# Kernel tuning notes

Measured on AMD Instinct MI355X. Metric: run time of the kernel, lower is better.

## Reference

```python
import jax, jax.numpy as jnp
import numpy as np
from jax import lax

N_HEADS = 8
D_KEYS = 128
HALF = D_KEYS // 2
N_KEYS = 256          # sub-keys per set; n_experts = N_KEYS**2
TOP_K = 8
D_MODEL = 512


def setup_inputs() -> dict:
    key = jax.random.key(0)
    ks = jax.random.split(key, 6)
    N, T = 2, 1024
    queries = jax.random.normal(ks[0], (N, T, D_MODEL), dtype=jnp.float32)
    Wq = jax.random.normal(ks[1], (D_MODEL, N_HEADS * D_KEYS), dtype=jnp.float32) / np.sqrt(D_MODEL)
    bq = jnp.zeros((N_HEADS * D_KEYS,), dtype=jnp.float32)
    bound = 1.0 / np.sqrt(HALF)
    keys = jax.random.uniform(ks[2], (N_HEADS, 2, N_KEYS, HALF), dtype=jnp.float32,
                              minval=-bound, maxval=bound)
    w_down = jax.random.normal(ks[3], (N_KEYS * N_KEYS, D_MODEL), dtype=jnp.float32) * 0.02
    w_up = jax.random.normal(ks[4], (N_KEYS * N_KEYS, D_MODEL), dtype=jnp.float32) * 0.02
    return {"queries": queries, "Wq": Wq, "bq": bq, "keys": keys,
            "w_down": w_down, "w_up": w_up}


def _forward(queries, Wq, bq, keys, w_down, w_up):
    N, T, D = queries.shape
    x = queries.reshape(-1, D)                                   # [B, D], B = N*T
    q = (x @ Wq + bq).reshape(-1, N_HEADS, D_KEYS)               # [B, H, d_keys]

    # product-key routing: score each half-query against each sub-key set
    q1, q2 = q[..., :HALF], q[..., HALF:]
    s1 = jnp.einsum('bhc,hnc->bhn', q1, keys[:, 0])              # [B, H, n_keys]
    s2 = jnp.einsum('bhc,hnc->bhn', q2, keys[:, 1])
    s1t, i1 = lax.top_k(s1, TOP_K)                               # [B, H, k]
    s2t, i2 = lax.top_k(s2, TOP_K)

    # cartesian product of the two top-k sets, then re-top-k
    all_scores = (s1t[..., :, None] + s2t[..., None, :]).reshape(-1, N_HEADS, TOP_K * TOP_K)
    all_idx = (i1[..., :, None] * N_KEYS + i2[..., None, :]).reshape(-1, N_HEADS, TOP_K * TOP_K)
    scores, best = lax.top_k(all_scores, TOP_K)                  # [B, H, k]
    indices = jnp.take_along_axis(all_idx, best, axis=-1)        # [B, H, k]

    # gather per-token expert weights and combine (PEER single-neuron experts)
    w_d = w_down[indices]                                        # [B, H, k, D]
    w_u = w_up[indices]                                          # [B, H, k, D]
    inner = jnp.einsum('bd,bhkd->bhk', x, w_d)                   # [B, H, k]
    vals = jax.nn.relu(inner) * jax.nn.softmax(scores, axis=-1)
    out = jnp.einsum('bhk,bhkd->bd', vals, w_u)                  # [B, D]
    return out.reshape(N, T, D)


def reference(queries, Wq, bq, keys, w_down, w_up):
    return _forward(queries, Wq, bq, keys, w_down, w_up)
```

## Files before the change

### kernel.cpp

```cpp
#include <hip/hip_runtime.h>
#include <math.h>

#define D_MODEL 512
#define NH      8
#define DK      128
#define HALFD   64
#define NKEYS   256
#define TOPK    8
#define NTOK    2048

__global__ __launch_bounds__(256) void qproj_gemm(const float* __restrict__ A,
                                                  const float* __restrict__ B,
                                                  const float* __restrict__ bias,
                                                  float* __restrict__ C) {
  const int N = NH * DK, K = D_MODEL;
  __shared__ float As[16][68];
  __shared__ float Bs[16][68];
  int tid = threadIdx.x;
  int tx = tid & 15, ty = tid >> 4;
  int m0 = blockIdx.y * 64, n0 = blockIdx.x * 64;
  float c[4][4];
#pragma unroll
  for (int i = 0; i < 4; ++i)
#pragma unroll
    for (int j = 0; j < 4; ++j) c[i][j] = 0.f;

  for (int k0 = 0; k0 < K; k0 += 16) {
    {
      int row = tid >> 2, kk = (tid & 3) << 2;
      float4 av = *(const float4*)(A + (size_t)(m0 + row) * K + k0 + kk);
      As[kk + 0][row] = av.x;
      As[kk + 1][row] = av.y;
      As[kk + 2][row] = av.z;
      As[kk + 3][row] = av.w;
    }
    {
      int kr = tid >> 4, nn = (tid & 15) << 2;
      *(float4*)&Bs[kr][nn] = *(const float4*)(B + (size_t)(k0 + kr) * N + n0 + nn);
    }
    __syncthreads();
#pragma unroll
    for (int k = 0; k < 16; ++k) {
      float4 a = *(const float4*)&As[k][ty << 2];
      float4 b = *(const float4*)&Bs[k][tx << 2];
      float av[4] = {a.x, a.y, a.z, a.w};
      float bv[4] = {b.x, b.y, b.z, b.w};
#pragma unroll
      for (int i = 0; i < 4; ++i)
#pragma unroll
        for (int j = 0; j < 4; ++j) c[i][j] += av[i] * bv[j];
    }
    __syncthreads();
  }
#pragma unroll
  for (int i = 0; i < 4; ++i) {
    int m = m0 + (ty << 2) + i;
#pragma unroll
    for (int j = 0; j < 4; ++j) {
      int n = n0 + (tx << 2) + j;
      C[(size_t)m * N + n] = c[i][j] + bias[n];
    }
  }
}

__global__ __launch_bounds__(256) void score_gemm(const float* __restrict__ qbuf,
                                                  const float* __restrict__ keys,
                                                  float* __restrict__ scores) {
  __shared__ float As[16][68];
  __shared__ float Bs[16][68];
  int tid = threadIdx.x;
  int tx = tid & 15, ty = tid >> 4;
  int n0 = blockIdx.x * 64, m0 = blockIdx.y * 64, slab = blockIdx.z;
  const float* Ap = qbuf + (size_t)slab * HALFD;
  const float* Bp = keys + (size_t)slab * NKEYS * HALFD;
  float c[4][4];
#pragma unroll
  for (int i = 0; i < 4; ++i)
#pragma unroll
    for (int j = 0; j < 4; ++j) c[i][j] = 0.f;

  for (int k0 = 0; k0 < HALFD; k0 += 16) {
    int row = tid >> 2, kk = (tid & 3) << 2;
    {
      float4 av = *(const float4*)(Ap + (size_t)(m0 + row) * (NH * DK) + k0 + kk);
      As[kk + 0][row] = av.x;
      As[kk + 1][row] = av.y;
      As[kk + 2][row] = av.z;
      As[kk + 3][row] = av.w;
    }
    {
      float4 bv = *(const float4*)(Bp + (size_t)(n0 + row) * HALFD + k0 + kk);
      Bs[kk + 0][row] = bv.x;
      Bs[kk + 1][row] = bv.y;
      Bs[kk + 2][row] = bv.z;
      Bs[kk + 3][row] = bv.w;
    }
    __syncthreads();
#pragma unroll
    for (int k = 0; k < 16; ++k) {
      float4 a = *(const float4*)&As[k][ty << 2];
      float4 b = *(const float4*)&Bs[k][tx << 2];
      float av[4] = {a.x, a.y, a.z, a.w};
      float bv[4] = {b.x, b.y, b.z, b.w};
#pragma unroll
      for (int i = 0; i < 4; ++i)
#pragma unroll
        for (int j = 0; j < 4; ++j) c[i][j] += av[i] * bv[j];
    }
    __syncthreads();
  }
#pragma unroll
  for (int i = 0; i < 4; ++i) {
    int m = m0 + (ty << 2) + i;
    float4 cv = make_float4(c[i][0], c[i][1], c[i][2], c[i][3]);
    *(float4*)&scores[((size_t)m * 16 + slab) * NKEYS + n0 + (tx << 2)] = cv;
  }
}

#define CE(a, b)                                                        \
  do {                                                                  \
    if (lv[a] < lv[b] || (lv[a] == lv[b] && li[a] > li[b])) {           \
      float tv_ = lv[a]; lv[a] = lv[b]; lv[b] = tv_;                    \
      int ti_ = li[a]; li[a] = li[b]; li[b] = ti_;                      \
    }                                                                   \
  } while (0)

__global__ __launch_bounds__(256) void topk_kernel(const float* __restrict__ scores,
                                                   int* __restrict__ widx,
                                                   float* __restrict__ wval) {
  int tid = threadIdx.x;
  int task = blockIdx.x * 4 + (tid >> 6);
  int ln = tid & 63;
  int b = task >> 3, h = task & 7;
  int s = ln >> 5, l = ln & 31;

  const float* sp = scores + ((size_t)b * 16 + h * 2 + s) * NKEYS + l * 8;
  float lv[8];
  int li[8];
  {
    float4 v0 = *(const float4*)sp;
    float4 v1 = *(const float4*)(sp + 4);
    lv[0] = v0.x; lv[1] = v0.y; lv[2] = v0.z; lv[3] = v0.w;
    lv[4] = v1.x; lv[5] = v1.y; lv[6] = v1.z; lv[7] = v1.w;
#pragma unroll
    for (int m = 0; m < 8; ++m) li[m] = l * 8 + m;
  }
  CE(0, 1); CE(2, 3); CE(0, 2); CE(1, 3); CE(1, 2);
  CE(4, 5); CE(6, 7); CE(4, 6); CE(5, 7); CE(5, 6);
  CE(0, 4); CE(1, 5); CE(2, 6); CE(3, 7);
  CE(2, 4); CE(3, 5);
  CE(1, 2); CE(3, 4); CE(5, 6);

  float wv_cap = 0.f;
  int wn_cap = 0;
#pragma unroll
  for (int k = 0; k < 8; ++k) {
    float v = lv[0];
    int n = li[0];
#pragma unroll
    for (int off = 16; off; off >>= 1) {
      float ov = __shfl_xor(v, off);
      int on = __shfl_xor(n, off);
      if (ov > v || (ov == v && on < n)) { v = ov; n = on; }
    }
    if (l == k) { wv_cap = v; wn_cap = n; }
    if (li[0] == n) {
#pragma unroll
      for (int m = 0; m < 7; ++m) { lv[m] = lv[m + 1]; li[m] = li[m + 1]; }
      lv[7] = -INFINITY;
      li[7] = 1 << 30;
    }
  }

  int i = ln >> 3, j = ln & 7;
  float v_i = __shfl(wv_cap, i);
  float v_j = __shfl(wv_cap, 32 + j);
  int n_i = __shfl(wn_cap, i);
  int n_j = __shfl(wn_cap, 32 + j);
  float cv = v_i + v_j;
  int ci = n_i * NKEYS + n_j;
  int p = ln;
#pragma unroll
  for (int k = 2; k <= 64; k <<= 1) {
#pragma unroll
    for (int j2 = k >> 1; j2 > 0; j2 >>= 1) {
      float ov = __shfl_xor(cv, j2);
      int op = __shfl_xor(p, j2);
      bool descBlock = ((ln & k) == 0);
      bool lower = ((ln & j2) == 0);
      bool mineBefore = (cv > ov) || (cv == ov && p < op);
      bool keep = (descBlock == lower) ? mineBefore : !mineBefore;
      if (!keep) { cv = ov; p = op; }
    }
  }
  float m0 = __shfl(cv, 0);
  float e = expf(cv - m0);
  float d = e;
#pragma unroll
  for (int off = 1; off < 8; off <<= 1) d += __shfl_xor(d, off);
  int wci = __shfl(ci, p);
  if (ln < TOPK) {
    size_t o = ((size_t)b * NH + h) * TOPK + ln;
    wval[o] = e / d;
    widx[o] = wci;
  }
}

__global__ __launch_bounds__(256) void gather_out(const float* __restrict__ x,
                                                  const float* __restrict__ w_down,
                                                  const float* __restrict__ w_up,
                                                  const int* __restrict__ widx,
                                                  const float* __restrict__ wval,
                                                  float* __restrict__ out) {
  int b = blockIdx.x;
  int tid = threadIdx.x;
  int ln = tid & 63, w = tid >> 6;
  __shared__ float lds_o[4][D_MODEL];

  const float4* xrow = (const float4*)(x + (size_t)b * D_MODEL);
  float4 x0 = xrow[ln * 2], x1 = xrow[ln * 2 + 1];
  float oa[8];
#pragma unroll
  for (int e = 0; e < 8; ++e) oa[e] = 0.f;

  for (int pp = 0; pp < 16; ++pp) {
    int pair = w * 16 + pp;
    int idx = widx[b * 64 + pair];
    float wt = wval[b * 64 + pair];
    const float4* wd = (const float4*)(w_down + (size_t)idx * D_MODEL);
    float4 d0 = wd[ln * 2], d1 = wd[ln * 2 + 1];
    float part = x0.x * d0.x + x0.y * d0.y + x0.z * d0.z + x0.w * d0.w +
                 x1.x * d1.x + x1.y * d1.y + x1.z * d1.z + x1.w * d1.w;
#pragma unroll
    for (int off = 32; off; off >>= 1) part += __shfl_xor(part, off);
    float val = fmaxf(part, 0.f) * wt;
    const float4* wu = (const float4*)(w_up + (size_t)idx * D_MODEL);
    float4 u0 = wu[ln * 2], u1 = wu[ln * 2 + 1];
    oa[0] += val * u0.x; oa[1] += val * u0.y; oa[2] += val * u0.z; oa[3] += val * u0.w;
    oa[4] += val * u1.x; oa[5] += val * u1.y; oa[6] += val * u1.z; oa[7] += val * u1.w;
  }
  *(float4*)&lds_o[w][ln * 8]     = make_float4(oa[0], oa[1], oa[2], oa[3]);
  *(float4*)&lds_o[w][ln * 8 + 4] = make_float4(oa[4], oa[5], oa[6], oa[7]);
  __syncthreads();
  for (int d = tid; d < D_MODEL; d += 256) {
    out[(size_t)b * D_MODEL + d] = lds_o[0][d] + lds_o[1][d] + lds_o[2][d] + lds_o[3][d];
  }
}

extern "C" void kernel_launch(void* const* d_in, const int* in_sizes, int n_in,
                              void* d_out, int out_size, void* d_ws, size_t ws_size,
                              hipStream_t stream) {
  const float* queries = (const float*)d_in[0];
  const float* Wq      = (const float*)d_in[1];
  const float* bq      = (const float*)d_in[2];
  const float* keys    = (const float*)d_in[3];
  const float* w_down  = (const float*)d_in[4];
  const float* w_up    = (const float*)d_in[5];
  float* outp = (float*)d_out;

  char* base = (char*)d_ws;
  float* qbuf   = (float*)base;
  float* scores = (float*)(base + (size_t)8 * 1024 * 1024);
  int*   widx   = (int*)(base + (size_t)42 * 1024 * 1024);
  float* wval   = (float*)(base + (size_t)43 * 1024 * 1024);

  qproj_gemm<<<dim3(16, 32), 256, 0, stream>>>(queries, Wq, bq, qbuf);
  score_gemm<<<dim3(4, 32, 16), 256, 0, stream>>>(qbuf, keys, scores);
  topk_kernel<<<4096, 256, 0, stream>>>(scores, widx, wval);
  gather_out<<<2048, 256, 0, stream>>>(queries, w_down, w_up, widx, wval, outp);
}
```

Baseline: 169.9 us.

## Split expert gather into value pass and sparse up-projection pass skipping zero relu

Splits the fused gather kernel into two kernels. The first computes relu(x·w_down)·softmax per selected expert, with each wave loading four w_down rows concurrently. The second accumulates w_up rows and skips experts whose value is zero, avoiding roughly half the w_up reads. This adds a kernel launch and a small intermediate buffer round trip, which reuses the q-projection workspace.

```diff
diff --git a/kernel.cpp b/kernel.cpp
--- a/kernel.cpp
+++ b/kernel.cpp
@@ -206,38 +206,80 @@
   }
 }
 
-__global__ __launch_bounds__(256) void gather_out(const float* __restrict__ x,
-                                                  const float* __restrict__ w_down,
-                                                  const float* __restrict__ w_up,
-                                                  const int* __restrict__ widx,
-                                                  const float* __restrict__ wval,
-                                                  float* __restrict__ out) {
+__global__ __launch_bounds__(256) void compute_vals(const float* __restrict__ x,
+                                                    const float* __restrict__ w_down,
+                                                    const int* __restrict__ widx,
+                                                    const float* __restrict__ wval,
+                                                    float* __restrict__ vals) {
+  int tid = threadIdx.x;
+  int ln = tid & 63;
+  int gw = blockIdx.x * 4 + (tid >> 6);
+  int b = gw >> 4;
+  int pbase = b * 64 + (gw & 15) * 4;
+
+  const float4* xr = (const float4*)(x + (size_t)b * D_MODEL);
+  float4 x0 = xr[ln * 2], x1 = xr[ln * 2 + 1];
+
+  int idx0 = widx[pbase + 0];
+  int idx1 = widx[pbase + 1];
+  int idx2 = widx[pbase + 2];
+  int idx3 = widx[pbase + 3];
+  const float4* r0 = (const float4*)(w_down + (size_t)idx0 * D_MODEL);
+  const float4* r1 = (const float4*)(w_down + (size_t)idx1 * D_MODEL);
+  const float4* r2 = (const float4*)(w_down + (size_t)idx2 * D_MODEL);
+  const float4* r3 = (const float4*)(w_down + (size_t)idx3 * D_MODEL);
+  float4 a0 = r0[ln * 2], b0 = r0[ln * 2 + 1];
+  float4 a1 = r1[ln * 2], b1 = r1[ln * 2 + 1];
+  float4 a2 = r2[ln * 2], b2 = r2[ln * 2 + 1];
+  float4 a3 = r3[ln * 2], b3 = r3[ln * 2 + 1];
+
+  float d0 = x0.x * a0.x + x0.y * a0.y + x0.z * a0.z + x0.w * a0.w +
+             x1.x * b0.x + x1.y * b0.y + x1.z * b0.z + x1.w * b0.w;
+  float d1 = x0.x * a1.x + x0.y * a1.y + x0.z * a1.z + x0.w * a1.w +
+             x1.x * b1.x + x1.y * b1.y + x1.z * b1.z + x1.w * b1.w;
+  float d2 = x0.x * a2.x + x0.y * a2.y + x0.z * a2.z + x0.w * a2.w +
+             x1.x * b2.x + x1.y * b2.y + x1.z * b2.z + x1.w * b2.w;
+  float d3 = x0.x * a3.x + x0.y * a3.y + x0.z * a3.z + x0.w * a3.w +
+             x1.x * b3.x + x1.y * b3.y + x1.z * b3.z + x1.w * b3.w;
+
+#pragma unroll
+  for (int off = 32; off; off >>= 1) {
+    d0 += __shfl_xor(d0, off);
+    d1 += __shfl_xor(d1, off);
+    d2 += __shfl_xor(d2, off);
+    d3 += __shfl_xor(d3, off);
+  }
+  if (ln == 0) {
+    vals[pbase + 0] = fmaxf(d0, 0.f) * wval[pbase + 0];
+    vals[pbase + 1] = fmaxf(d1, 0.f) * wval[pbase + 1];
+    vals[pbase + 2] = fmaxf(d2, 0.f) * wval[pbase + 2];
+    vals[pbase + 3] = fmaxf(d3, 0.f) * wval[pbase + 3];
+  }
+}
+
+__global__ __launch_bounds__(256) void accum_out(const float* __restrict__ w_up,
+                                                 const int* __restrict__ widx,
+                                                 const float* __restrict__ vals,
+                                                 float* __restrict__ out) {
   int b = blockIdx.x;
   int tid = threadIdx.x;
   int ln = tid & 63, w = tid >> 6;
   __shared__ float lds_o[4][D_MODEL];
 
-  const float4* xrow = (const float4*)(x + (size_t)b * D_MODEL);
-  float4 x0 = xrow[ln * 2], x1 = xrow[ln * 2 + 1];
   float oa[8];
 #pragma unroll
   for (int e = 0; e < 8; ++e) oa[e] = 0.f;
 
   for (int pp = 0; pp < 16; ++pp) {
-    int pair = w * 16 + pp;
-    int idx = widx[b * 64 + pair];
-    float wt = wval[b * 64 + pair];
-    const float4* wd = (const float4*)(w_down + (size_t)idx * D_MODEL);
-    float4 d0 = wd[ln * 2], d1 = wd[ln * 2 + 1];
-    float part = x0.x * d0.x + x0.y * d0.y + x0.z * d0.z + x0.w * d0.w +
-                 x1.x * d1.x + x1.y * d1.y + x1.z * d1.z + x1.w * d1.w;
-#pragma unroll
-    for (int off = 32; off; off >>= 1) part += __shfl_xor(part, off);
-    float val = fmaxf(part, 0.f) * wt;
-    const float4* wu = (const float4*)(w_up + (size_t)idx * D_MODEL);
-    float4 u0 = wu[ln * 2], u1 = wu[ln * 2 + 1];
-    oa[0] += val * u0.x; oa[1] += val * u0.y; oa[2] += val * u0.z; oa[3] += val * u0.w;
-    oa[4] += val * u1.x; oa[5] += val * u1.y; oa[6] += val * u1.z; oa[7] += val * u1.w;
+    int pair = b * 64 + w * 16 + pp;
+    float val = vals[pair];
+    if (val > 0.f) {
+      int idx = widx[pair];
+      const float4* wu = (const float4*)(w_up + (size_t)idx * D_MODEL);
+      float4 u0 = wu[ln * 2], u1 = wu[ln * 2 + 1];
+      oa[0] += val * u0.x; oa[1] += val * u0.y; oa[2] += val * u0.z; oa[3] += val * u0.w;
+      oa[4] += val * u1.x; oa[5] += val * u1.y; oa[6] += val * u1.z; oa[7] += val * u1.w;
+    }
   }
   *(float4*)&lds_o[w][ln * 8]     = make_float4(oa[0], oa[1], oa[2], oa[3]);
   *(float4*)&lds_o[w][ln * 8 + 4] = make_float4(oa[4], oa[5], oa[6], oa[7]);
@@ -263,9 +305,11 @@
   float* scores = (float*)(base + (size_t)8 * 1024 * 1024);
   int*   widx   = (int*)(base + (size_t)42 * 1024 * 1024);
   float* wval   = (float*)(base + (size_t)43 * 1024 * 1024);
+  float* vals   = (float*)base;
 
   qproj_gemm<<<dim3(16, 32), 256, 0, stream>>>(queries, Wq, bq, qbuf);
   score_gemm<<<dim3(4, 32, 16), 256, 0, stream>>>(qbuf, keys, scores);
   topk_kernel<<<4096, 256, 0, stream>>>(scores, widx, wval);
-  gather_out<<<2048, 256, 0, stream>>>(queries, w_down, w_up, widx, wval, outp);
-}
+  compute_vals<<<8192, 256, 0, stream>>>(queries, w_down, widx, wval, vals);
+  accum_out<<<2048, 256, 0, stream>>>(w_up, widx, vals, outp);
+}
```

Measured after the change: 151.8 us. -10.6%, faster.

## Split expert gather into batched down-projection and ReLU-skipping up-accumulation kernels

Applied to the files above, without the earlier changes.

The fused gather kernel becomes two kernels. compute_vals issues eight independent w_down row loads per wave so more memory requests are in flight, then writes the ReLU-and-softmax-weighted values to a buffer that reuses the qbuf region. accum_out uses 512 threads and skips the w_up row load for any pair whose value is non-positive, which cuts gather traffic for roughly half the experts. The q-projection GEMM also moves to 128-row tiles with vectorized bias and stores. In exchange there is an extra launch and an extra pass through global memory for vals.

```diff
diff --git a/kernel.cpp b/kernel.cpp
--- a/kernel.cpp
+++ b/kernel.cpp
@@ -14,20 +14,22 @@
                                                   const float* __restrict__ bias,
                                                   float* __restrict__ C) {
   const int N = NH * DK, K = D_MODEL;
-  __shared__ float As[16][68];
+  __shared__ float As[16][132];
   __shared__ float Bs[16][68];
   int tid = threadIdx.x;
   int tx = tid & 15, ty = tid >> 4;
-  int m0 = blockIdx.y * 64, n0 = blockIdx.x * 64;
-  float c[4][4];
-#pragma unroll
-  for (int i = 0; i < 4; ++i)
+  int m0 = blockIdx.y * 128, n0 = blockIdx.x * 64;
+  float c[8][4];
+#pragma unroll
+  for (int i = 0; i < 8; ++i)
 #pragma unroll
     for (int j = 0; j < 4; ++j) c[i][j] = 0.f;
 
   for (int k0 = 0; k0 < K; k0 += 16) {
-    {
-      int row = tid >> 2, kk = (tid & 3) << 2;
+#pragma unroll
+    for (int rep = 0; rep < 2; ++rep) {
+      int row = (tid >> 2) + rep * 64;
+      int kk = (tid & 3) << 2;
       float4 av = *(const float4*)(A + (size_t)(m0 + row) * K + k0 + kk);
       As[kk + 0][row] = av.x;
       As[kk + 1][row] = av.y;
@@ -41,25 +43,24 @@
     __syncthreads();
 #pragma unroll
     for (int k = 0; k < 16; ++k) {
-      float4 a = *(const float4*)&As[k][ty << 2];
+      float4 a0 = *(const float4*)&As[k][ty << 3];
+      float4 a1 = *(const float4*)&As[k][(ty << 3) + 4];
       float4 b = *(const float4*)&Bs[k][tx << 2];
-      float av[4] = {a.x, a.y, a.z, a.w};
+      float av[8] = {a0.x, a0.y, a0.z, a0.w, a1.x, a1.y, a1.z, a1.w};
       float bv[4] = {b.x, b.y, b.z, b.w};
 #pragma unroll
-      for (int i = 0; i < 4; ++i)
+      for (int i = 0; i < 8; ++i)
 #pragma unroll
         for (int j = 0; j < 4; ++j) c[i][j] += av[i] * bv[j];
     }
     __syncthreads();
   }
-#pragma unroll
-  for (int i = 0; i < 4; ++i) {
-    int m = m0 + (ty << 2) + i;
-#pragma unroll
-    for (int j = 0; j < 4; ++j) {
-      int n = n0 + (tx << 2) + j;
-      C[(size_t)m * N + n] = c[i][j] + bias[n];
-    }
+  float4 bb = *(const float4*)&bias[n0 + (tx << 2)];
+#pragma unroll
+  for (int i = 0; i < 8; ++i) {
+    int m = m0 + (ty << 3) + i;
+    float4 cv = make_float4(c[i][0] + bb.x, c[i][1] + bb.y, c[i][2] + bb.z, c[i][3] + bb.w);
+    *(float4*)&C[(size_t)m * N + n0 + (tx << 2)] = cv;
   }
 }
 
@@ -206,44 +207,82 @@
   }
 }
 
-__global__ __launch_bounds__(256) void gather_out(const float* __restrict__ x,
-                                                  const float* __restrict__ w_down,
-                                                  const float* __restrict__ w_up,
-                                                  const int* __restrict__ widx,
-                                                  const float* __restrict__ wval,
-                                                  float* __restrict__ out) {
+__global__ __launch_bounds__(256) void compute_vals(const float* __restrict__ x,
+                                                    const float* __restrict__ w_down,
+                                                    const int* __restrict__ widx,
+                                                    const float* __restrict__ wval,
+                                                    float* __restrict__ vals) {
+  int tid = threadIdx.x;
+  int ln = tid & 63;
+  int gw = blockIdx.x * 4 + (tid >> 6);
+  int b = gw >> 3;
+  int pbase = b * 64 + (gw & 7) * 8;
+
+  const float4* xr = (const float4*)(x + (size_t)b * D_MODEL);
+  float4 x0 = xr[ln * 2], x1 = xr[ln * 2 + 1];
+
+  int idx[8];
+#pragma unroll
+  for (int r = 0; r < 8; ++r) idx[r] = widx[pbase + r];
+
+  float4 ra[8], rb[8];
+#pragma unroll
+  for (int r = 0; r < 8; ++r) {
+    const float4* rp = (const float4*)(w_down + (size_t)idx[r] * D_MODEL);
+    ra[r] = rp[ln * 2];
+    rb[r] = rp[ln * 2 + 1];
+  }
+
+  float d[8];
+#pragma unroll
+  for (int r = 0; r < 8; ++r) {
+    d[r] = x0.x * ra[r].x + x0.y * ra[r].y + x0.z * ra[r].z + x0.w * ra[r].w +
+           x1.x * rb[r].x + x1.y * rb[r].y + x1.z * rb[r].z + x1.w * rb[r].w;
+  }
+#pragma unroll
+  for (int off = 32; off; off >>= 1) {
+#pragma unroll
+    for (int r = 0; r < 8; ++r) d[r] += __shfl_xor(d[r], off);
+  }
+  if (ln == 0) {
+#pragma unroll
+    for (int r = 0; r < 8; ++r)
+      vals[pbase + r] = fmaxf(d[r], 0.f) * wval[pbase + r];
+  }
+}
+
+__global__ __launch_bounds__(512) void accum_out(const float* __restrict__ w_up,
+                                                 const int* __restrict__ widx,
+                                                 const float* __restrict__ vals,
+                                                 float* __restrict__ out) {
   int b = blockIdx.x;
   int tid = threadIdx.x;
   int ln = tid & 63, w = tid >> 6;
-  __shared__ float lds_o[4][D_MODEL];
-
-  const float4* xrow = (const float4*)(x + (size_t)b * D_MODEL);
-  float4 x0 = xrow[ln * 2], x1 = xrow[ln * 2 + 1];
+  __shared__ float lds_o[8][D_MODEL];
+
   float oa[8];
 #pragma unroll
   for (int e = 0; e < 8; ++e) oa[e] = 0.f;
 
-  for (int pp = 0; pp < 16; ++pp) {
-    int pair = w * 16 + pp;
-    int idx = widx[b * 64 + pair];
-    float wt = wval[b * 64 + pair];
-    const float4* wd = (const float4*)(w_down + (size_t)idx * D_MODEL);
-    float4 d0 = wd[ln * 2], d1 = wd[ln * 2 + 1];
-    float part = x0.x * d0.x + x0.y * d0.y + x0.z * d0.z + x0.w * d0.w +
-                 x1.x * d1.x + x1.y * d1.y + x1.z * d1.z + x1.w * d1.w;
-#pragma unroll
-    for (int off = 32; off; off >>= 1) part += __shfl_xor(part, off);
-    float val = fmaxf(part, 0.f) * wt;
-    const float4* wu = (const float4*)(w_up + (size_t)idx * D_MODEL);
-    float4 u0 = wu[ln * 2], u1 = wu[ln * 2 + 1];
-    oa[0] += val * u0.x; oa[1] += val * u0.y; oa[2] += val * u0.z; oa[3] += val * u0.w;
-    oa[4] += val * u1.x; oa[5] += val * u1.y; oa[6] += val * u1.z; oa[7] += val * u1.w;
+  for (int pp = 0; pp < 8; ++pp) {
+    int pair = b * 64 + w * 8 + pp;
+    float val = vals[pair];
+    if (val > 0.f) {
+      int idx = widx[pair];
+      const float4* wu = (const float4*)(w_up + (size_t)idx * D_MODEL);
+      float4 u0 = wu[ln * 2], u1 = wu[ln * 2 + 1];
+      oa[0] += val * u0.x; oa[1] += val * u0.y; oa[2] += val * u0.z; oa[3] += val * u0.w;
+      oa[4] += val * u1.x; oa[5] += val * u1.y; oa[6] += val * u1.z; oa[7] += val * u1.w;
+    }
   }
   *(float4*)&lds_o[w][ln * 8]     = make_float4(oa[0], oa[1], oa[2], oa[3]);
   *(float4*)&lds_o[w][ln * 8 + 4] = make_float4(oa[4], oa[5], oa[6], oa[7]);
   __syncthreads();
-  for (int d = tid; d < D_MODEL; d += 256) {
-    out[(size_t)b * D_MODEL + d] = lds_o[0][d] + lds_o[1][d] + lds_o[2][d] + lds_o[3][d];
+  {
+    int d = tid;
+    float acc = lds_o[0][d] + lds_o[1][d] + lds_o[2][d] + lds_o[3][d] +
+                lds_o[4][d] + lds_o[5][d] + lds_o[6][d] + lds_o[7][d];
+    out[(size_t)b * D_MODEL + d] = acc;
   }
 }
 
@@ -263,9 +302,11 @@
   float* scores = (float*)(base + (size_t)8 * 1024 * 1024);
   int*   widx   = (int*)(base + (size_t)42 * 1024 * 1024);
   float* wval   = (float*)(base + (size_t)43 * 1024 * 1024);
-
-  qproj_gemm<<<dim3(16, 32), 256, 0, stream>>>(queries, Wq, bq, qbuf);
+  float* vals   = (float*)base;
+
+  qproj_gemm<<<dim3(16, 16), 256, 0, stream>>>(queries, Wq, bq, qbuf);
   score_gemm<<<dim3(4, 32, 16), 256, 0, stream>>>(qbuf, keys, scores);
   topk_kernel<<<4096, 256, 0, stream>>>(scores, widx, wval);
-  gather_out<<<2048, 256, 0, stream>>>(queries, w_down, w_up, widx, wval, outp);
-}
+  compute_vals<<<4096, 256, 0, stream>>>(queries, w_down, widx, wval, vals);
+  accum_out<<<2048, 512, 0, stream>>>(w_up, widx, vals, outp);
+}
```

After: 168.9 us. No clear change (-0.6%).
